# Performance work log

Hardware: AMD Instinct MI355X
Metric: run time of the kernel (lower is better)

Reference implementation:

```python
import jax, jax.numpy as jnp
import numpy as np

NUM_GRAPHS = 512  # number of segments (graphs) in the batch
NEG_SLOPE = 0.01  # nn.LeakyReLU default


def setup_inputs() -> dict:
    key = jax.random.key(0)
    k1, k2, k3, k4, k5 = jax.random.split(key, 5)
    N, D = 200000, 128
    h_topo = jax.random.normal(k1, (N, D), dtype=jnp.float32)
    h_geom = jax.random.normal(k2, (N, D), dtype=jnp.float32)
    batch = jnp.sort(jax.random.randint(k3, (N,), 0, NUM_GRAPHS, dtype=jnp.int64))
    concat_dim, hidden, out_dim = 6 * D, 2 * D, 128
    W1 = jax.random.normal(k4, (concat_dim, hidden), dtype=jnp.float32) * 0.02
    b1 = jnp.zeros((hidden,), dtype=jnp.float32)
    W2 = jax.random.normal(k5, (hidden, out_dim), dtype=jnp.float32) * 0.02
    b2 = jnp.zeros((out_dim,), dtype=jnp.float32)
    return {"h_topo": h_topo, "h_geom": h_geom, "batch": batch,
            "W1": W1, "b1": b1, "W2": W2, "b2": b2}


def _pool_feats(h, batch):
    # global_max_pool / global_mean_pool keyed by graph id, gathered back per node
    gmax = jax.ops.segment_max(h, batch, num_segments=NUM_GRAPHS)
    gsum = jax.ops.segment_sum(h, batch, num_segments=NUM_GRAPHS)
    cnt = jax.ops.segment_sum(jnp.ones((h.shape[0],), h.dtype), batch,
                              num_segments=NUM_GRAPHS)
    gmean = gsum / jnp.maximum(cnt, 1.0)[:, None]
    return gmax[batch], gmean[batch]  # [N, D] each


def reference(h_topo, h_geom, batch, W1, b1, W2, b2):
    t_max, t_mean = _pool_feats(h_topo, batch)
    g_max, g_mean = _pool_feats(h_geom, batch)
    # [Topo, Geom, TopoMax, TopoMean, GeomMax, GeomMean]
    combined = jnp.concatenate(
        [h_topo, t_max, t_mean, h_geom, g_max, g_mean], axis=-1)  # [N, 6D]
    h = combined @ W1 + b1
    h = jnp.where(h >= 0, h, NEG_SLOPE * h)  # LeakyReLU
    return h @ W2 + b2
```

## Files before the change

### kernel.cpp

```cpp
#include <hip/hip_runtime.h>
#include <math.h>

#define NUM_GRAPHS 512
#define D 128
#define NEG 0.01f
#define BN 128
#define NS 4

typedef __attribute__((ext_vector_type(8))) short  bf16x8;
typedef __attribute__((ext_vector_type(4))) float  f32x4;
typedef __attribute__((ext_vector_type(4))) int    i32x4;

__device__ __forceinline__ unsigned short f2bf(float f) {
    unsigned u = __float_as_uint(f);
    u += 0x7fffu + ((u >> 16) & 1u);
    return (unsigned short)(u >> 16);
}

__device__ __forceinline__ bf16x8 cvt8(float4 a, float4 b) {
    unsigned w0, w1, w2, w3;
    asm("v_cvt_pk_bf16_f32 %0, %1, %2" : "=v"(w0) : "v"(a.x), "v"(a.y));
    asm("v_cvt_pk_bf16_f32 %0, %1, %2" : "=v"(w1) : "v"(a.z), "v"(a.w));
    asm("v_cvt_pk_bf16_f32 %0, %1, %2" : "=v"(w2) : "v"(b.x), "v"(b.y));
    asm("v_cvt_pk_bf16_f32 %0, %1, %2" : "=v"(w3) : "v"(b.z), "v"(b.w));
    i32x4 v; v[0] = (int)w0; v[1] = (int)w1; v[2] = (int)w2; v[3] = (int)w3;
    return __builtin_bit_cast(bf16x8, v);
}

__device__ __forceinline__ int swz128(int row, int k) {
    return (row >> 6) * 16384 + (row & 63) * 256 + (k ^ ((row & 7) << 3));
}

#define LDS_BARRIER()                                                        \
    do {                                                                     \
        asm volatile("s_waitcnt lgkmcnt(0)" ::: "memory");                   \
        __builtin_amdgcn_s_barrier();                                        \
        asm volatile("" ::: "memory");                                       \
    } while (0)

#define FMAX4(a, b)                                                          \
    do {                                                                     \
        (a).x = fmaxf((a).x, (b).x); (a).y = fmaxf((a).y, (b).y);            \
        (a).z = fmaxf((a).z, (b).z); (a).w = fmaxf((a).w, (b).w);            \
    } while (0)
#define FADD4(a, b)                                                          \
    do {                                                                     \
        (a).x += (b).x; (a).y += (b).y; (a).z += (b).z; (a).w += (b).w;      \
    } while (0)

__global__ __launch_bounds__(256) void bounds_kernel(
    const int* __restrict__ batch, int N, int* __restrict__ seg)
{
    const int g = blockIdx.x * 256 + threadIdx.x;
    if (g <= NUM_GRAPHS) {
        int lo = 0, hi = N;
        while (lo < hi) { int m = (lo + hi) >> 1; if (batch[m] < g) lo = m + 1; else hi = m; }
        seg[g] = lo;
    }
}

__global__ __launch_bounds__(256) void pool_kernel(
    const float* __restrict__ h_topo, const float* __restrict__ h_geom,
    const int* __restrict__ seg, int N, float* __restrict__ pp)
{
    const int g = blockIdx.x, t = blockIdx.y, s = blockIdx.z;
    const float* __restrict__ h = t ? h_geom : h_topo;

    const int start = seg[g], end = seg[g + 1];
    const int len = end - start;
    const int r0  = start + (int)(((long long)len * s) / NS);
    const int r1  = start + (int)(((long long)len * (s + 1)) / NS);

    const int c = threadIdx.x & 31;
    const int r = threadIdx.x >> 5;

    float4 mxA = make_float4(-INFINITY, -INFINITY, -INFINITY, -INFINITY);
    float4 mxB = mxA, mxC = mxA, mxD = mxA;
    float4 smA = make_float4(0.f, 0.f, 0.f, 0.f);
    float4 smB = smA, smC = smA, smD = smA;

    int row = r0 + r;
    for (; row + 24 < r1; row += 32) {
        float4 v0 = *(const float4*)(h + (size_t)row * D + c * 4);
        float4 v1 = *(const float4*)(h + (size_t)(row + 8)  * D + c * 4);
        float4 v2 = *(const float4*)(h + (size_t)(row + 16) * D + c * 4);
        float4 v3 = *(const float4*)(h + (size_t)(row + 24) * D + c * 4);
        FMAX4(mxA, v0); FADD4(smA, v0);
        FMAX4(mxB, v1); FADD4(smB, v1);
        FMAX4(mxC, v2); FADD4(smC, v2);
        FMAX4(mxD, v3); FADD4(smD, v3);
    }
    for (; row < r1; row += 8) {
        float4 v = *(const float4*)(h + (size_t)row * D + c * 4);
        FMAX4(mxA, v); FADD4(smA, v);
    }
    FMAX4(mxA, mxB); FMAX4(mxC, mxD); FMAX4(mxA, mxC);
    FADD4(smA, smB); FADD4(smC, smD); FADD4(smA, smC);

    __shared__ float4 smx[256], ssm[256];
    smx[threadIdx.x] = mxA; ssm[threadIdx.x] = smA;
    __syncthreads();
    #pragma unroll
    for (int st = 4; st > 0; st >>= 1) {
        if (r < st) {
            float4 a = smx[threadIdx.x + st * 32];
            float4 b = ssm[threadIdx.x + st * 32];
            float4 m0 = smx[threadIdx.x];
            float4 s0 = ssm[threadIdx.x];
            FMAX4(m0, a); FADD4(s0, b);
            smx[threadIdx.x] = m0; ssm[threadIdx.x] = s0;
        }
        __syncthreads();
    }
    if (r == 0) {
        float* dst = pp + ((size_t)(g * 2 + t) * NS + s) * 256;
        *(float4*)(dst + c * 4)       = smx[threadIdx.x];
        *(float4*)(dst + 128 + c * 4) = ssm[threadIdx.x];
    }
}

__global__ __launch_bounds__(256) void pmat_kernel(
    const float* __restrict__ pp, const int* __restrict__ seg,
    const float* __restrict__ W1, const float* __restrict__ b1,
    float* __restrict__ P)
{
    const int g = blockIdx.x;
    const int j = threadIdx.x;

    const int start = seg[g], end = seg[g + 1];
    const float inv   = 1.0f / fmaxf((float)(end - start), 1.0f);
    const bool  empty = (end <= start);

    __shared__ float pl[512];
    #pragma unroll
    for (int e0 = 0; e0 < 2; ++e0) {
        const int e = j + e0 * 256;
        const int t = e >> 8, i = e & 255;
        const float* q = pp + (size_t)(g * 2 + t) * NS * 256 + i;
        float v;
        if (i < 128)
            v = fmaxf(fmaxf(q[0], q[256]), fmaxf(q[512], q[768]));
        else
            v = (q[0] + q[256] + q[512] + q[768]) * inv;
        pl[e] = empty ? 0.f : v;
    }
    __syncthreads();

    float acc = b1[j];
    #pragma unroll 8
    for (int k = 0; k < 256; ++k)
        acc += pl[k] * W1[(size_t)(128 + k) * 256 + j];
    #pragma unroll 8
    for (int k = 0; k < 256; ++k)
        acc += pl[256 + k] * W1[(size_t)(512 + k) * 256 + j];

    P[(size_t)g * 256 + j] = acc;
}

__global__ __launch_bounds__(256) void wconv_kernel(
    const float* __restrict__ W1, const float* __restrict__ W2,
    unsigned short* __restrict__ W1bT, unsigned short* __restrict__ W2bT)
{
    const int idx = blockIdx.x * 256 + threadIdx.x;
    if (idx < 256 * 256) {
        const int n = idx >> 8, k = idx & 255;
        const int kk = (k < 128) ? k : (k + 256);
        W1bT[idx] = f2bf(W1[(size_t)kk * 256 + n]);
    } else {
        const int j = idx - 256 * 256;
        if (j < 128 * 256) {
            const int n = j >> 8, k = j & 255;
            W2bT[j] = f2bf(W2[(size_t)k * 128 + n]);
        }
    }
}

__global__ __launch_bounds__(512, 4) void mlp_mfma(
    const float* __restrict__ h_topo, const float* __restrict__ h_geom,
    const int* __restrict__ batch, const float* __restrict__ P,
    const unsigned short* __restrict__ W1bT, const unsigned short* __restrict__ W2bT,
    const float* __restrict__ b2, float* __restrict__ out, int N)
{
    __shared__ unsigned short xs[128 * 256];
    __shared__ int gid[128];

    const int tid  = threadIdx.x;
    const int wave = tid >> 6, lane = tid & 63;
    const int base = (gridDim.x - 1 - blockIdx.x) * BN;

    {
        const int row  = tid >> 2, kq = tid & 3;
        const int node = min(base + row, N - 1);
        const float* src = (kq < 2) ? h_topo + (size_t)node * D + kq * 64
                                    : h_geom + (size_t)node * D + (kq - 2) * 64;
        #pragma unroll
        for (int i = 0; i < 8; ++i) {
            float4 a = ((const float4*)src)[2 * i];
            float4 b = ((const float4*)src)[2 * i + 1];
            *(bf16x8*)&xs[swz128(row, kq * 64 + i * 8)] = cvt8(a, b);
        }
    }
    if (tid < 128) gid[tid] = batch[min(base + tid, N - 1)];

    const int g0 = batch[base];
    const int g1 = batch[min(base + 127, N - 1)];
    const bool uni = (g0 == g1);

    const int lhi = lane >> 4;
    const int llo = lane & 15;

    const unsigned short* w1p = W1bT + (size_t)(wave * 32 + llo) * 256 + lhi * 8;

    float pf[2];
    if (uni) {
        #pragma unroll
        for (int ct = 0; ct < 2; ++ct)
            pf[ct] = P[(size_t)g0 * 256 + wave * 32 + ct * 16 + llo];
    }

    bf16x8 bfr[2][2];
    #pragma unroll
    for (int ct = 0; ct < 2; ++ct) {
        bfr[0][ct] = *(const bf16x8*)(w1p + (size_t)ct * 16 * 256);
        bfr[1][ct] = *(const bf16x8*)(w1p + (size_t)ct * 16 * 256 + 32);
    }

    LDS_BARRIER();

    f32x4 acc[8][2];
    #pragma unroll
    for (int rt = 0; rt < 8; ++rt)
        #pragma unroll
        for (int ct = 0; ct < 2; ++ct) {
            const float p = uni ? pf[ct] : 0.f;
            acc[rt][ct] = (f32x4){p, p, p, p};
        }

    #pragma unroll
    for (int ks = 0; ks < 8; ++ks) {
        const int kb = ks * 32 + lhi * 8;
        bf16x8 afr[8];
        #pragma unroll
        for (int rt = 0; rt < 8; ++rt)
            afr[rt] = *(const bf16x8*)&xs[swz128(rt * 16 + llo, kb)];
        __builtin_amdgcn_s_setprio(1);
        #pragma unroll
        for (int rt = 0; rt < 8; ++rt)
            #pragma unroll
            for (int ct = 0; ct < 2; ++ct)
                acc[rt][ct] = __builtin_amdgcn_mfma_f32_16x16x32_bf16(
                    afr[rt], bfr[ks & 1][ct], acc[rt][ct], 0, 0, 0);
        __builtin_amdgcn_s_setprio(0);
        if (ks < 6) {
            const int kbn = (ks + 2) * 32;
            #pragma unroll
            for (int ct = 0; ct < 2; ++ct)
                bfr[ks & 1][ct] = *(const bf16x8*)(w1p + (size_t)ct * 16 * 256 + kbn);
        }
    }

    const int jp = wave & 3, ng = wave >> 2;
    const unsigned short* w2pA = W2bT + (size_t)((2 * jp)     * 16 + llo) * 256 + lhi * 8;
    const unsigned short* w2pB = W2bT + (size_t)((2 * jp + 1) * 16 + llo) * 256 + lhi * 8;

    bf16x8 bfr2[2][2];
    bfr2[0][0] = *(const bf16x8*)(w2pA);
    bfr2[0][1] = *(const bf16x8*)(w2pB);
    bfr2[1][0] = *(const bf16x8*)(w2pA + 32);
    bfr2[1][1] = *(const bf16x8*)(w2pB + 32);

    LDS_BARRIER();

    #pragma unroll
    for (int rt = 0; rt < 8; ++rt) {
        #pragma unroll
        for (int ct = 0; ct < 2; ++ct) {
            const int col = wave * 32 + ct * 16 + llo;
            #pragma unroll
            for (int q = 0; q < 4; ++q) {
                const int row = rt * 16 + lhi * 4 + q;
                float v = acc[rt][ct][q];
                if (!uni) v += P[(size_t)gid[row] * 256 + col];
                v = fmaxf(v, NEG * v);
                xs[swz128(row, col)] = f2bf(v);
            }
        }
    }

    LDS_BARRIER();

    f32x4 acc2[4][2];
    {
        const float4 bbA = *(const float4*)(b2 + (2 * jp)     * 16 + lhi * 4);
        const float4 bbB = *(const float4*)(b2 + (2 * jp + 1) * 16 + lhi * 4);
        #pragma unroll
        for (int nt = 0; nt < 4; ++nt) {
            acc2[nt][0] = (f32x4){bbA.x, bbA.y, bbA.z, bbA.w};
            acc2[nt][1] = (f32x4){bbB.x, bbB.y, bbB.z, bbB.w};
        }
    }
    #pragma unroll
    for (int ks = 0; ks < 8; ++ks) {
        const int kb = ks * 32 + lhi * 8;
        bf16x8 hfr[4];
        #pragma unroll
        for (int nt = 0; nt < 4; ++nt)
            hfr[nt] = *(const bf16x8*)&xs[swz128((ng * 4 + nt) * 16 + llo, kb)];
        __builtin_amdgcn_s_setprio(1);
        #pragma unroll
        for (int nt = 0; nt < 4; ++nt) {
            acc2[nt][0] = __builtin_amdgcn_mfma_f32_16x16x32_bf16(
                bfr2[ks & 1][0], hfr[nt], acc2[nt][0], 0, 0, 0);
            acc2[nt][1] = __builtin_amdgcn_mfma_f32_16x16x32_bf16(
                bfr2[ks & 1][1], hfr[nt], acc2[nt][1], 0, 0, 0);
        }
        __builtin_amdgcn_s_setprio(0);
        if (ks < 6) {
            bfr2[ks & 1][0] = *(const bf16x8*)(w2pA + (ks + 2) * 32);
            bfr2[ks & 1][1] = *(const bf16x8*)(w2pB + (ks + 2) * 32);
        }
    }

    #pragma unroll
    for (int nt = 0; nt < 4; ++nt) {
        const int node = base + (ng * 4 + nt) * 16 + llo;
        if (node < N) {
            float* op = out + (size_t)node * 128 + jp * 32 + lhi * 4;
            __builtin_nontemporal_store(acc2[nt][0], (f32x4*)op);
            __builtin_nontemporal_store(acc2[nt][1], (f32x4*)(op + 16));
        }
    }
}

extern "C" void kernel_launch(void* const* d_in, const int* in_sizes, int n_in,
                              void* d_out, int out_size, void* d_ws, size_t ws_size,
                              hipStream_t stream)
{
    const float* h_topo = (const float*)d_in[0];
    const float* h_geom = (const float*)d_in[1];
    const int*   batch  = (const int*)  d_in[2];
    const float* W1     = (const float*)d_in[3];
    const float* b1     = (const float*)d_in[4];
    const float* W2     = (const float*)d_in[5];
    const float* b2     = (const float*)d_in[6];
    float* out = (float*)d_out;

    const int N = in_sizes[0] / D;

    float*          pp   = (float*)d_ws;
    float*          P    = pp + (size_t)NUM_GRAPHS * 2 * NS * 256;
    unsigned short* W1bT = (unsigned short*)(P + (size_t)NUM_GRAPHS * 256);
    unsigned short* W2bT = W1bT + 256 * 256;
    int*            seg  = (int*)(W2bT + 128 * 256);

    bounds_kernel<<<3, 256, 0, stream>>>(batch, N, seg);
    wconv_kernel<<<(256 * 256 + 128 * 256) / 256, 256, 0, stream>>>(W1, W2, W1bT, W2bT);
    pool_kernel<<<dim3(NUM_GRAPHS, 2, NS), 256, 0, stream>>>(h_topo, h_geom, seg, N, pp);
    pmat_kernel<<<NUM_GRAPHS, 256, 0, stream>>>(pp, seg, W1, b1, P);

    const int nblocks = (N + BN - 1) / BN;
    mlp_mfma<<<nblocks, 512, 0, stream>>>(h_topo, h_geom, batch, P,
                                          W1bT, W2bT, b2, out, N);
}
```

Measured before the change: 175.2 us.

## Retile first GEMM to 2x4 wave grid with transposed MFMA operands

The first GEMM is now split across the 8 waves as a 2x4 grid of 64x64 tiles instead of each wave covering all 128 rows by 32 columns. The MFMA operand order is swapped so weights act as A and node features as B. This halves LDS fragment reads per wave and lets the epilogue add the pooled bias with float4 loads and write packed bf16 pairs. The second GEMM's wave mapping is adjusted to match. It raises W1 register use (4 column tiles double-buffered) and may change LDS bank-conflict patterns.

```diff
diff --git a/kernel.cpp b/kernel.cpp
--- a/kernel.cpp
+++ b/kernel.cpp
@@ -209,81 +209,90 @@
     const int lhi = lane >> 4;
     const int llo = lane & 15;
 
-    const unsigned short* w1p = W1bT + (size_t)(wave * 32 + llo) * 256 + lhi * 8;
-
-    float pf[2];
+    const int wr = wave >> 2, wc = wave & 3;
+
+    const unsigned short* w1p = W1bT + (size_t)(wc * 64 + llo) * 256 + lhi * 8;
+
+    float4 pf4[4];
     if (uni) {
         #pragma unroll
-        for (int ct = 0; ct < 2; ++ct)
-            pf[ct] = P[(size_t)g0 * 256 + wave * 32 + ct * 16 + llo];
-    }
-
-    bf16x8 bfr[2][2];
-    #pragma unroll
-    for (int ct = 0; ct < 2; ++ct) {
-        bfr[0][ct] = *(const bf16x8*)(w1p + (size_t)ct * 16 * 256);
-        bfr[1][ct] = *(const bf16x8*)(w1p + (size_t)ct * 16 * 256 + 32);
+        for (int ct = 0; ct < 4; ++ct)
+            pf4[ct] = *(const float4*)(P + (size_t)g0 * 256 + wc * 64 + ct * 16 + lhi * 4);
+    }
+
+    bf16x8 aW[2][4];
+    #pragma unroll
+    for (int ct = 0; ct < 4; ++ct) {
+        aW[0][ct] = *(const bf16x8*)(w1p + (size_t)ct * 16 * 256);
+        aW[1][ct] = *(const bf16x8*)(w1p + (size_t)ct * 16 * 256 + 32);
     }
 
     LDS_BARRIER();
 
-    f32x4 acc[8][2];
-    #pragma unroll
-    for (int rt = 0; rt < 8; ++rt)
-        #pragma unroll
-        for (int ct = 0; ct < 2; ++ct) {
-            const float p = uni ? pf[ct] : 0.f;
-            acc[rt][ct] = (f32x4){p, p, p, p};
-        }
+    f32x4 acc[4][4];
+    #pragma unroll
+    for (int rt = 0; rt < 4; ++rt)
+        #pragma unroll
+        for (int ct = 0; ct < 4; ++ct)
+            acc[rt][ct] = uni ? (f32x4){pf4[ct].x, pf4[ct].y, pf4[ct].z, pf4[ct].w}
+                              : (f32x4){0.f, 0.f, 0.f, 0.f};
 
     #pragma unroll
     for (int ks = 0; ks < 8; ++ks) {
         const int kb = ks * 32 + lhi * 8;
-        bf16x8 afr[8];
-        #pragma unroll
-        for (int rt = 0; rt < 8; ++rt)
-            afr[rt] = *(const bf16x8*)&xs[swz128(rt * 16 + llo, kb)];
+        bf16x8 bX[4];
+        #pragma unroll
+        for (int rt = 0; rt < 4; ++rt)
+            bX[rt] = *(const bf16x8*)&xs[swz128(wr * 64 + rt * 16 + llo, kb)];
         __builtin_amdgcn_s_setprio(1);
         #pragma unroll
-        for (int rt = 0; rt < 8; ++rt)
+        for (int rt = 0; rt < 4; ++rt)
             #pragma unroll
-            for (int ct = 0; ct < 2; ++ct)
+            for (int ct = 0; ct < 4; ++ct)
                 acc[rt][ct] = __builtin_amdgcn_mfma_f32_16x16x32_bf16(
-                    afr[rt], bfr[ks & 1][ct], acc[rt][ct], 0, 0, 0);
+                    aW[ks & 1][ct], bX[rt], acc[rt][ct], 0, 0, 0);
         __builtin_amdgcn_s_setprio(0);
         if (ks < 6) {
             const int kbn = (ks + 2) * 32;
             #pragma unroll
-            for (int ct = 0; ct < 2; ++ct)
-                bfr[ks & 1][ct] = *(const bf16x8*)(w1p + (size_t)ct * 16 * 256 + kbn);
-        }
-    }
-
-    const int jp = wave & 3, ng = wave >> 2;
-    const unsigned short* w2pA = W2bT + (size_t)((2 * jp)     * 16 + llo) * 256 + lhi * 8;
-    const unsigned short* w2pB = W2bT + (size_t)((2 * jp + 1) * 16 + llo) * 256 + lhi * 8;
-
-    bf16x8 bfr2[2][2];
-    bfr2[0][0] = *(const bf16x8*)(w2pA);
-    bfr2[0][1] = *(const bf16x8*)(w2pB);
-    bfr2[1][0] = *(const bf16x8*)(w2pA + 32);
-    bfr2[1][1] = *(const bf16x8*)(w2pB + 32);
+            for (int ct = 0; ct < 4; ++ct)
+                aW[ks & 1][ct] = *(const bf16x8*)(w1p + (size_t)ct * 16 * 256 + kbn);
+        }
+    }
+
+    const int wr2 = wave >> 2, wc2 = wave & 3;
+    const unsigned short* w2pA = W2bT + (size_t)(wc2 * 32 + llo) * 256 + lhi * 8;
+    const unsigned short* w2pB = W2bT + (size_t)(wc2 * 32 + 16 + llo) * 256 + lhi * 8;
+
+    bf16x8 aW2[2][2];
+    aW2[0][0] = *(const bf16x8*)(w2pA);
+    aW2[0][1] = *(const bf16x8*)(w2pB);
+    aW2[1][0] = *(const bf16x8*)(w2pA + 32);
+    aW2[1][1] = *(const bf16x8*)(w2pB + 32);
 
     LDS_BARRIER();
 
     #pragma unroll
-    for (int rt = 0; rt < 8; ++rt) {
-        #pragma unroll
-        for (int ct = 0; ct < 2; ++ct) {
-            const int col = wave * 32 + ct * 16 + llo;
-            #pragma unroll
-            for (int q = 0; q < 4; ++q) {
-                const int row = rt * 16 + lhi * 4 + q;
-                float v = acc[rt][ct][q];
-                if (!uni) v += P[(size_t)gid[row] * 256 + col];
-                v = fmaxf(v, NEG * v);
-                xs[swz128(row, col)] = f2bf(v);
+    for (int rt = 0; rt < 4; ++rt) {
+        const int nrow = wr * 64 + rt * 16 + llo;
+        int gg = 0;
+        if (!uni) gg = gid[nrow];
+        #pragma unroll
+        for (int ct = 0; ct < 4; ++ct) {
+            const int j0 = wc * 64 + ct * 16 + lhi * 4;
+            float4 v = make_float4(acc[rt][ct][0], acc[rt][ct][1],
+                                   acc[rt][ct][2], acc[rt][ct][3]);
+            if (!uni) {
+                float4 pv = *(const float4*)(P + (size_t)gg * 256 + j0);
+                v.x += pv.x; v.y += pv.y; v.z += pv.z; v.w += pv.w;
             }
+            v.x = fmaxf(v.x, NEG * v.x); v.y = fmaxf(v.y, NEG * v.y);
+            v.z = fmaxf(v.z, NEG * v.z); v.w = fmaxf(v.w, NEG * v.w);
+            unsigned w0, w1;
+            asm("v_cvt_pk_bf16_f32 %0, %1, %2" : "=v"(w0) : "v"(v.x), "v"(v.y));
+            asm("v_cvt_pk_bf16_f32 %0, %1, %2" : "=v"(w1) : "v"(v.z), "v"(v.w));
+            uint2 hw; hw.x = w0; hw.y = w1;
+            *(uint2*)&xs[swz128(nrow, j0)] = hw;
         }
     }
 
@@ -291,8 +300,8 @@
 
     f32x4 acc2[4][2];
     {
-        const float4 bbA = *(const float4*)(b2 + (2 * jp)     * 16 + lhi * 4);
-        const float4 bbB = *(const float4*)(b2 + (2 * jp + 1) * 16 + lhi * 4);
+        const float4 bbA = *(const float4*)(b2 + wc2 * 32 + lhi * 4);
+        const float4 bbB = *(const float4*)(b2 + wc2 * 32 + 16 + lhi * 4);
         #pragma unroll
         for (int nt = 0; nt < 4; ++nt) {
             acc2[nt][0] = (f32x4){bbA.x, bbA.y, bbA.z, bbA.w};
@@ -302,30 +311,30 @@
     #pragma unroll
     for (int ks = 0; ks < 8; ++ks) {
         const int kb = ks * 32 + lhi * 8;
-        bf16x8 hfr[4];
+        bf16x8 bH[4];
         #pragma unroll
         for (int nt = 0; nt < 4; ++nt)
-            hfr[nt] = *(const bf16x8*)&xs[swz128((ng * 4 + nt) * 16 + llo, kb)];
+            bH[nt] = *(const bf16x8*)&xs[swz128(wr2 * 64 + nt * 16 + llo, kb)];
         __builtin_amdgcn_s_setprio(1);
         #pragma unroll
         for (int nt = 0; nt < 4; ++nt) {
             acc2[nt][0] = __builtin_amdgcn_mfma_f32_16x16x32_bf16(
-                bfr2[ks & 1][0], hfr[nt], acc2[nt][0], 0, 0, 0);
+                aW2[ks & 1][0], bH[nt], acc2[nt][0], 0, 0, 0);
             acc2[nt][1] = __builtin_amdgcn_mfma_f32_16x16x32_bf16(
-                bfr2[ks & 1][1], hfr[nt], acc2[nt][1], 0, 0, 0);
+                aW2[ks & 1][1], bH[nt], acc2[nt][1], 0, 0, 0);
         }
         __builtin_amdgcn_s_setprio(0);
         if (ks < 6) {
-            bfr2[ks & 1][0] = *(const bf16x8*)(w2pA + (ks + 2) * 32);
-            bfr2[ks & 1][1] = *(const bf16x8*)(w2pB + (ks + 2) * 32);
+            aW2[ks & 1][0] = *(const bf16x8*)(w2pA + (ks + 2) * 32);
+            aW2[ks & 1][1] = *(const bf16x8*)(w2pB + (ks + 2) * 32);
         }
     }
 
     #pragma unroll
     for (int nt = 0; nt < 4; ++nt) {
-        const int node = base + (ng * 4 + nt) * 16 + llo;
+        const int node = base + wr2 * 64 + nt * 16 + llo;
         if (node < N) {
-            float* op = out + (size_t)node * 128 + jp * 32 + lhi * 4;
+            float* op = out + (size_t)node * 128 + wc2 * 32 + lhi * 4;
             __builtin_nontemporal_store(acc2[nt][0], (f32x4*)op);
             __builtin_nontemporal_store(acc2[nt][1], (f32x4*)(op + 16));
         }
```

New measurement: 194.0 us. +10.7%, slower.
